# Optimization experiments

Measured on AMD Instinct MI355X. Metric: run time of the kernel, lower is better.

The kernel has to match this reference:

```python
import jax, jax.numpy as jnp
import numpy as np
from jax import lax

B, T, C, K = 16, 1024, 512, 5
PAD = (K - 1) // 2
EPS_LN = 1e-5
EPS_BN = 1e-5


def setup_inputs() -> dict:
    key = jax.random.key(0)
    ks = jax.random.split(key, 8)
    s1 = 1.0 / np.sqrt(C)          # fan-in of pointwise conv1 (C -> 2C)
    s2 = 1.0 / np.sqrt(2 * C * K)  # fan-in of k=5 conv (2C -> 2C)
    s3 = 1.0 / np.sqrt(C)          # fan-in of pointwise conv3 (C -> C)
    return {
        "x": jax.random.normal(ks[0], (B, T, C), jnp.float32),
        "ln_g": jnp.ones((C,), jnp.float32),
        "ln_b": jnp.zeros((C,), jnp.float32),
        "w1": (jax.random.normal(ks[1], (2 * C, C), jnp.float32) * s1),
        "b1": jnp.zeros((2 * C,), jnp.float32),
        "w2": (jax.random.normal(ks[2], (K, 2 * C, 2 * C), jnp.float32) * s2),  # WIO layout
        "b2": jnp.zeros((2 * C,), jnp.float32),
        "bn_g": jnp.ones((C,), jnp.float32),
        "bn_b": jnp.zeros((C,), jnp.float32),
        "bn_mean": jax.random.normal(ks[3], (C,), jnp.float32) * 0.1,
        "bn_var": jax.random.uniform(ks[4], (C,), jnp.float32, 0.5, 1.5),
        "w3": (jax.random.normal(ks[5], (C, C), jnp.float32) * s3),
        "b3": jnp.zeros((C,), jnp.float32),
    }


def reference(x, ln_g, ln_b, w1, b1, w2, b2, bn_g, bn_b, bn_mean, bn_var, w3, b3):
    # LayerNorm over channel dim (B, T, C)
    mu = jnp.mean(x, axis=-1, keepdims=True)
    var = jnp.mean(jnp.square(x - mu), axis=-1, keepdims=True)
    h = (x - mu) * lax.rsqrt(var + EPS_LN) * ln_g + ln_b

    # pointwise conv C -> 2C (kernel 1 == GEMM), then Swish
    h = jnp.einsum('btc,oc->bto', h, w1) + b1        # (B, T, 2C)
    h = h * jax.nn.sigmoid(h)

    # kernel-5 conv 2C -> 2C, 'same' padding, channels-last
    h = lax.conv_general_dilated(
        h, w2, window_strides=(1,), padding=[(PAD, PAD)],
        dimension_numbers=('NWC', 'WIO', 'NWC')) + b2  # (B, T, 2C)

    # GLU over channel dim: first half * sigmoid(second half)
    a, g = h[..., :C], h[..., C:]
    h = a * jax.nn.sigmoid(g)                        # (B, T, C)

    # BatchNorm1d(C), eval mode (running stats)
    h = (h - bn_mean) * lax.rsqrt(bn_var + EPS_BN) * bn_g + bn_b

    # pointwise conv C -> C; dropout is identity at inference.
    # Torch output is sequential(...)(B,C,T).transpose(1,2) -> (B, T, C)
    return jnp.einsum('btc,oc->bto', h, w3) + b3
```

## Files before the change

kernel.cpp:

```cpp
#include <hip/hip_runtime.h>
#include <cstdint>


#define NB    16
#define TT    1024
#define CC    512
#define C2    1024
#define TPAD  1028

typedef unsigned short u16;
typedef short bf16x8 __attribute__((ext_vector_type(8)));
typedef float f32x4  __attribute__((ext_vector_type(4)));
typedef __attribute__((address_space(3))) u16 lds_u16;
typedef const __attribute__((address_space(1))) u16 glb_u16;

__device__ __forceinline__ float bf2f(u16 u) {
  union { unsigned int i; float f; } v; v.i = ((unsigned int)u) << 16; return v.f;
}
__device__ __forceinline__ u16 f2bf(float f) {
  union { float f; unsigned int i; } v; v.f = f;
  unsigned int x = v.i;
  return (u16)((x + 0x7fffu + ((x >> 16) & 1u)) >> 16);
}

__global__ __launch_bounds__(256) void prep_k(
    const float* __restrict__ w1, u16* __restrict__ w1b,
    const float* __restrict__ w3, u16* __restrict__ w3b,
    u16* __restrict__ h1p) {
  const int b = blockIdx.x;
  if (b < 512) {
    const int i = (b * 256 + threadIdx.x) * 4;
    float4 v = *(const float4*)(w1 + i);
    u16 o[4] = { f2bf(v.x), f2bf(v.y), f2bf(v.z), f2bf(v.w) };
    *(uint2*)(w1b + i) = *(const uint2*)o;
  } else if (b < 768) {
    const int i = ((b - 512) * 256 + threadIdx.x) * 4;
    float4 v = *(const float4*)(w3 + i);
    u16 o[4] = { f2bf(v.x), f2bf(v.y), f2bf(v.z), f2bf(v.w) };
    *(uint2*)(w3b + i) = *(const uint2*)o;
  } else {
    const int idx = (b - 768) * 256 + threadIdx.x;
    const int bb  = idx >> 9;
    const int rem = idx & 511;
    const int ri  = rem >> 7;
    const int c8  = (rem & 127) * 8;
    const int row = bb * TPAD + (ri < 2 ? ri : 1024 + ri);
    uint4 z = make_uint4(0u, 0u, 0u, 0u);
    *(uint4*)(h1p + (size_t)row * C2 + c8) = z;
  }
}

__global__ void transpose_w2(const float* __restrict__ w2, u16* __restrict__ w2t) {
  __shared__ u16 t[64][65];
  const int k  = blockIdx.z;
  const int i0 = blockIdx.x * 64, o0 = blockIdx.y * 64;
  const int tx = threadIdx.x, ty = threadIdx.y;
  for (int r = ty; r < 64; r += 4)
    t[r][tx] = f2bf(w2[((size_t)(k * C2) + i0 + r) * C2 + o0 + tx]);
  __syncthreads();
  for (int r = ty; r < 64; r += 4)
    w2t[((size_t)(k * C2) + o0 + r) * C2 + i0 + tx] = t[tx][r];
}

__global__ __launch_bounds__(256) void layernorm_k(
    const float* __restrict__ x, const float* __restrict__ lng,
    const float* __restrict__ lnb, u16* __restrict__ out) {
  const int tok  = blockIdx.x * 4 + (threadIdx.x >> 6);
  const int lane = threadIdx.x & 63;
  const float* xp = x + (size_t)tok * CC + lane * 8;
  float f[8];
  *(float4*)(f)     = *(const float4*)(xp);
  *(float4*)(f + 4) = *(const float4*)(xp + 4);
  float s = 0.f, s2 = 0.f;
#pragma unroll
  for (int j = 0; j < 8; j++) { s += f[j]; s2 += f[j] * f[j]; }
#pragma unroll
  for (int m = 32; m >= 1; m >>= 1) { s += __shfl_xor(s, m, 64); s2 += __shfl_xor(s2, m, 64); }
  const float mu  = s  * (1.f / 512.f);
  const float var = s2 * (1.f / 512.f) - mu * mu;
  const float rs  = rsqrtf(var + 1e-5f);
  u16 ov[8];
#pragma unroll
  for (int j = 0; j < 8; j++) {
    const int c = lane * 8 + j;
    ov[j] = f2bf((f[j] - mu) * rs * lng[c] + lnb[c]);
  }
  *(uint4*)(out + (size_t)tok * CC + lane * 8) = *(const uint4*)ov;
}

template <int EPI>
__global__ __launch_bounds__(256, 3) void gemm_bt(
    const u16* __restrict__ A, const u16* __restrict__ Bt,
    const float* __restrict__ bias, void* __restrict__ outv,
    const int Kd, const int ldA) {
  __shared__ __align__(16) u16 smem[20480];
  const int tid  = threadIdx.x;
  const int m0   = blockIdx.x * 128;
  const int n0   = blockIdx.y * 128;
  const int wave = tid >> 6, lane = tid & 63;
  const int wm = (wave & 1) * 64, wn = (wave >> 1) * 64;
  const int quad = lane >> 4, l16 = lane & 15;
  const int row = tid >> 2;
  const int kc  = (tid & 3) * 8;
  const int J = Kd >> 5;

  const u16* Ap0 = A + (size_t)(m0 + row) * ldA + kc;
  const u16* Ap1 = Ap0 + (size_t)64 * ldA;
  const u16* Bp0 = Bt + (size_t)(n0 + row) * Kd + kc;
  const u16* Bp1 = Bp0 + (size_t)64 * Kd;

  f32x4 acc[4][4] = {};
  uint4 rA0 = *(const uint4*)Ap0, rA1 = *(const uint4*)Ap1;
  uint4 rB0 = *(const uint4*)Bp0, rB1 = *(const uint4*)Bp1;
  *(uint4*)(smem + row * 40 + kc)                = rA0;
  *(uint4*)(smem + (64 + row) * 40 + kc)         = rA1;
  *(uint4*)(smem + 10240 + row * 40 + kc)        = rB0;
  *(uint4*)(smem + 10240 + (64 + row) * 40 + kc) = rB1;
  rA0 = *(const uint4*)(Ap0 + 32); rA1 = *(const uint4*)(Ap1 + 32);
  rB0 = *(const uint4*)(Bp0 + 32); rB1 = *(const uint4*)(Bp1 + 32);
  __syncthreads();

#pragma unroll 1
  for (int j = 0; j < J; j++) {
    const u16* curA = smem + (j & 1) * 5120;
    const u16* curB = smem + 10240 + (j & 1) * 5120;
    if (j + 1 < J) {
      u16* nxtA = smem + ((j + 1) & 1) * 5120;
      u16* nxtB = smem + 10240 + ((j + 1) & 1) * 5120;
      *(uint4*)(nxtA + row * 40 + kc)        = rA0;
      *(uint4*)(nxtA + (64 + row) * 40 + kc) = rA1;
      *(uint4*)(nxtB + row * 40 + kc)        = rB0;
      *(uint4*)(nxtB + (64 + row) * 40 + kc) = rB1;
    }
    {
      const int k2 = (j + 2 < J) ? (j + 2) * 32 : 0;
      rA0 = *(const uint4*)(Ap0 + k2); rA1 = *(const uint4*)(Ap1 + k2);
      rB0 = *(const uint4*)(Bp0 + k2); rB1 = *(const uint4*)(Bp1 + k2);
    }
    bf16x8 af[4], bfr[4];
#pragma unroll
    for (int i = 0; i < 4; i++)
      af[i] = *(const bf16x8*)(curA + (wm + i * 16 + l16) * 40 + quad * 8);
#pragma unroll
    for (int i = 0; i < 4; i++)
      bfr[i] = *(const bf16x8*)(curB + (wn + i * 16 + l16) * 40 + quad * 8);
#pragma unroll
    for (int mi = 0; mi < 4; mi++)
#pragma unroll
      for (int ni = 0; ni < 4; ni++)
        acc[mi][ni] = __builtin_amdgcn_mfma_f32_16x16x32_bf16(
            af[mi], bfr[ni], acc[mi][ni], 0, 0, 0);
    __syncthreads();
  }

  float bv[4];
#pragma unroll
  for (int ni = 0; ni < 4; ni++) bv[ni] = bias[n0 + wn + ni * 16 + l16];

  if (EPI == 0) {
    u16* epi = smem + wave * 4608;
#pragma unroll
    for (int mi = 0; mi < 4; mi++)
#pragma unroll
      for (int ni = 0; ni < 4; ni++)
#pragma unroll
        for (int r = 0; r < 4; r++) {
          float v = acc[mi][ni][r] + bv[ni];
          v = v / (1.f + __expf(-v));
          epi[(mi * 16 + quad * 4 + r) * 72 + ni * 16 + l16] = f2bf(v);
        }
    u16* h1p = (u16*)outv;
#pragma unroll
    for (int p = 0; p < 8; p++) {
      const int rrow = p * 8 + (lane >> 3);
      const int colb = (lane & 7) * 8;
      uint4 v = *(const uint4*)(epi + rrow * 72 + colb);
      const int rr = m0 + wm + rrow;
      const int bb = rr >> 10, tt = rr & 1023;
      *(uint4*)(h1p + (size_t)(bb * TPAD + tt + 2) * C2 + n0 + wn + colb) = v;
    }
  } else {
    float* fepi = (float*)(smem + wave * 4608);
    float* outf = (float*)outv;
#pragma unroll
    for (int mi = 0; mi < 4; mi++) {
      float* fp = fepi + (mi & 1) * 1088;
#pragma unroll
      for (int ni = 0; ni < 4; ni++)
#pragma unroll
        for (int r = 0; r < 4; r++)
          fp[(quad * 4 + r) * 68 + ni * 16 + l16] = acc[mi][ni][r] + bv[ni];
#pragma unroll
      for (int p = 0; p < 4; p++) {
        const int rrow = p * 4 + (lane >> 4);
        const int col  = (lane & 15) * 4;
        float4 v = *(const float4*)(fp + rrow * 68 + col);
        *(float4*)(outf + (size_t)(m0 + wm + mi * 16 + rrow) * CC + n0 + wn + col) = v;
      }
    }
  }
}

__global__ __launch_bounds__(256, 2) void conv5_mfma(
    const u16* __restrict__ h1p, const u16* __restrict__ w2t,
    const float* __restrict__ b2,
    const float* __restrict__ bng, const float* __restrict__ bnb,
    const float* __restrict__ bnm, const float* __restrict__ bnv,
    u16* __restrict__ h2) {
  __shared__ __align__(16) u16 smem[30880];
  const int tid = threadIdx.x;
  const int mt  = blockIdx.x;
  const int ya  = blockIdx.y * 64;
  const int bb  = mt >> 2;
  const int t0  = (mt & 3) * 256;
  const size_t arow0 = (size_t)bb * TPAD + t0;
  const int wave = tid >> 6, lane = tid & 63;
  const int wm = (wave & 1) * 128, wn = (wave >> 1) * 64;
  const int quad = lane >> 4, l16 = lane & 15;
  const int row = tid >> 2;
  const int kc  = (tid & 3) * 8;
  u16* lsB = smem + 10400;

  const u16* Ap0 = h1p + (arow0 + row) * C2 + kc;
  const u16* Ap1 = Ap0 + (size_t)64 * C2;
  const u16* Ap2 = Ap0 + (size_t)128 * C2;
  const u16* Ap3 = Ap0 + (size_t)192 * C2;
  const u16* Ap4 = h1p + (arow0 + 256 + row) * C2 + kc;

  const u16* Bb0 = w2t + (size_t)(ya + wave * 16 + (lane & 15)) * C2 + (lane >> 4) * 8;
  const u16* Bb1 = w2t + (size_t)(512 + ya + wave * 16 + (lane & 15)) * C2 + (lane >> 4) * 8;

  f32x4 acc[8][4] = {};
  uint4 rA0, rA1, rA2, rA3, rA4;

#define BG(PTR, T5, GQ, I0)                                                    \
  __builtin_amdgcn_global_load_lds(                                            \
      (glb_u16*)((PTR) + (size_t)(T5) * C2 * C2 + (I0)),                       \
      (lds_u16*)(lsB + ((T5) * 8 + (GQ)) * 512), 16, 0, 0);

  rA0 = *(const uint4*)Ap0; rA1 = *(const uint4*)Ap1;
  rA2 = *(const uint4*)Ap2; rA3 = *(const uint4*)Ap3;
  if (tid < 16) rA4 = *(const uint4*)Ap4;

#pragma unroll 1
  for (int j = 0; j < 32; j++) {
    __syncthreads();
    {
      const int ib0 = j * 32;
#pragma unroll
      for (int t5 = 0; t5 < 5; t5++) {
        BG(Bb0, t5, wave, ib0)
        BG(Bb1, t5, wave + 4, ib0)
      }
    }
    *(uint4*)(smem + row * 40 + kc)         = rA0;
    *(uint4*)(smem + (64 + row) * 40 + kc)  = rA1;
    *(uint4*)(smem + (128 + row) * 40 + kc) = rA2;
    *(uint4*)(smem + (192 + row) * 40 + kc) = rA3;
    if (tid < 16) *(uint4*)(smem + (256 + row) * 40 + kc) = rA4;
    __syncthreads();
    {
      const int ia = (j + 1 < 32) ? (j + 1) * 32 : 0;
      rA0 = *(const uint4*)(Ap0 + ia);
      rA1 = *(const uint4*)(Ap1 + ia);
      rA2 = *(const uint4*)(Ap2 + ia);
      rA3 = *(const uint4*)(Ap3 + ia);
      if (tid < 16) rA4 = *(const uint4*)(Ap4 + ia);
    }
#pragma unroll
    for (int k = 0; k < 5; k++) {
      bf16x8 bfr[4];
#pragma unroll
      for (int i = 0; i < 4; i++)
        bfr[i] = *(const bf16x8*)(lsB + (k * 8 + (wn >> 4) + i) * 512 + lane * 8);
#pragma unroll
      for (int h = 0; h < 2; h++) {
        bf16x8 af[4];
#pragma unroll
        for (int i = 0; i < 4; i++)
          af[i] = *(const bf16x8*)(smem + (wm + (h * 4 + i) * 16 + l16 + k) * 40 + quad * 8);
#pragma unroll
        for (int mi = 0; mi < 4; mi++)
#pragma unroll
          for (int ni = 0; ni < 4; ni++)
            acc[h * 4 + mi][ni] = __builtin_amdgcn_mfma_f32_16x16x32_bf16(
                af[mi], bfr[ni], acc[h * 4 + mi][ni], 0, 0, 0);
      }
    }
  }
#undef BG
  __syncthreads();

  float bv[4];
#pragma unroll
  for (int ni = 0; ni < 4; ni++)
    bv[ni] = b2[(wn >> 6) * 512 + ya + ni * 16 + l16];

  const int cb8 = (lane & 7) * 8;
  float sc8[8], bm8[8], bb8[8];
#pragma unroll
  for (int jj = 0; jj < 8; jj++) {
    const int c = ya + cb8 + jj;
    sc8[jj] = bng[c] * rsqrtf(bnv[c] + 1e-5f);
    bm8[jj] = bnm[c];
    bb8[jj] = bnb[c];
  }

  u16* abuf = smem;
  u16* gbuf = smem + 9216;
  const size_t orow0 = (size_t)bb * TT + t0;
#pragma unroll 1
  for (int hh = 0; hh < 2; hh++) {
    if ((wave & 1) == hh) {
      u16* buf = (wn >> 6) ? gbuf : abuf;
#pragma unroll
      for (int mi = 0; mi < 8; mi++)
#pragma unroll
        for (int ni = 0; ni < 4; ni++)
#pragma unroll
          for (int r = 0; r < 4; r++)
            buf[(mi * 16 + quad * 4 + r) * 72 + ni * 16 + l16] =
                f2bf(acc[mi][ni][r] + bv[ni]);
    }
    __syncthreads();
#pragma unroll
    for (int p = 0; p < 4; p++) {
      const int rr = wave * 32 + p * 8 + (lane >> 3);
      uint4 va = *(const uint4*)(abuf + rr * 72 + cb8);
      uint4 vg = *(const uint4*)(gbuf + rr * 72 + cb8);
      u16 aa[8], gg[8], oo[8];
      *(uint4*)aa = va; *(uint4*)gg = vg;
#pragma unroll
      for (int jj = 0; jj < 8; jj++) {
        const float a = bf2f(aa[jj]);
        const float g = bf2f(gg[jj]);
        const float h = a / (1.f + __expf(-g));
        oo[jj] = f2bf((h - bm8[jj]) * sc8[jj] + bb8[jj]);
      }
      *(uint4*)(h2 + (orow0 + hh * 128 + rr) * CC + ya + cb8) = *(const uint4*)oo;
    }
    __syncthreads();
  }
}

extern "C" void kernel_launch(void* const* d_in, const int* in_sizes, int n_in,
                              void* d_out, int out_size, void* d_ws, size_t ws_size,
                              hipStream_t stream) {
  const float* x   = (const float*)d_in[0];
  const float* lng = (const float*)d_in[1];
  const float* lnb = (const float*)d_in[2];
  const float* w1  = (const float*)d_in[3];
  const float* b1  = (const float*)d_in[4];
  const float* w2  = (const float*)d_in[5];
  const float* b2  = (const float*)d_in[6];
  const float* bng = (const float*)d_in[7];
  const float* bnb = (const float*)d_in[8];
  const float* bnm = (const float*)d_in[9];
  const float* bnv = (const float*)d_in[10];
  const float* w3  = (const float*)d_in[11];
  const float* b3  = (const float*)d_in[12];

  u16* ws  = (u16*)d_ws;
  u16* hln = ws;
  u16* h2  = hln;
  u16* h1p = ws + 8388608;
  u16* w2t = h1p + 16842752;
  u16* hcv = w2t + 5242880;
  u16* w1b = hcv + 16777216;
  u16* w3b = w1b + 524288;

  prep_k      <<<800, 256, 0, stream>>>(w1, w1b, w3, w3b, h1p);
  transpose_w2<<<dim3(16, 16, 5), dim3(64, 4), 0, stream>>>(w2, w2t);
  layernorm_k <<<4096, 256, 0, stream>>>(x, lng, lnb, hln);
  gemm_bt<0>  <<<dim3(128, 8), 256, 0, stream>>>(hln, w1b, b1, h1p, 512, 512);
  conv5_mfma  <<<dim3(64, 8), 256, 0, stream>>>(h1p, w2t, b2, bng, bnb, bnm, bnv, h2);
  gemm_bt<1>  <<<dim3(128, 4), 256, 0, stream>>>(h2, w3b, b3, d_out, 512, 512);
}
```

Measured before the change: 310.3 us.

## Merge prep, w2 transpose and layernorm into one launch; add dedicated SiLU GEMM

After: 312.7 us. About the same (+0.8%).

```diff
diff --git a/kernel.cpp b/kernel.cpp
--- a/kernel.cpp
+++ b/kernel.cpp
@@ -23,23 +23,28 @@
   return (u16)((x + 0x7fffu + ((x >> 16) & 1u)) >> 16);
 }
 
-__global__ __launch_bounds__(256) void prep_k(
+__global__ __launch_bounds__(256) void preproc_k(
     const float* __restrict__ w1, u16* __restrict__ w1b,
     const float* __restrict__ w3, u16* __restrict__ w3b,
-    u16* __restrict__ h1p) {
-  const int b = blockIdx.x;
+    u16* __restrict__ h1p,
+    const float* __restrict__ w2, u16* __restrict__ w2t,
+    const float* __restrict__ x, const float* __restrict__ lng,
+    const float* __restrict__ lnb, u16* __restrict__ hln) {
+  __shared__ u16 t[64][65];
+  const int b   = blockIdx.x;
+  const int tid = threadIdx.x;
   if (b < 512) {
-    const int i = (b * 256 + threadIdx.x) * 4;
+    const int i = (b * 256 + tid) * 4;
     float4 v = *(const float4*)(w1 + i);
     u16 o[4] = { f2bf(v.x), f2bf(v.y), f2bf(v.z), f2bf(v.w) };
     *(uint2*)(w1b + i) = *(const uint2*)o;
   } else if (b < 768) {
-    const int i = ((b - 512) * 256 + threadIdx.x) * 4;
+    const int i = ((b - 512) * 256 + tid) * 4;
     float4 v = *(const float4*)(w3 + i);
     u16 o[4] = { f2bf(v.x), f2bf(v.y), f2bf(v.z), f2bf(v.w) };
     *(uint2*)(w3b + i) = *(const uint2*)o;
-  } else {
-    const int idx = (b - 768) * 256 + threadIdx.x;
+  } else if (b < 800) {
+    const int idx = (b - 768) * 256 + tid;
     const int bb  = idx >> 9;
     const int rem = idx & 511;
     const int ri  = rem >> 7;
@@ -47,45 +52,145 @@
     const int row = bb * TPAD + (ri < 2 ? ri : 1024 + ri);
     uint4 z = make_uint4(0u, 0u, 0u, 0u);
     *(uint4*)(h1p + (size_t)row * C2 + c8) = z;
-  }
-}
-
-__global__ void transpose_w2(const float* __restrict__ w2, u16* __restrict__ w2t) {
-  __shared__ u16 t[64][65];
-  const int k  = blockIdx.z;
-  const int i0 = blockIdx.x * 64, o0 = blockIdx.y * 64;
-  const int tx = threadIdx.x, ty = threadIdx.y;
-  for (int r = ty; r < 64; r += 4)
-    t[r][tx] = f2bf(w2[((size_t)(k * C2) + i0 + r) * C2 + o0 + tx]);
+  } else if (b < 2080) {
+    const int bt = b - 800;
+    const int k  = bt >> 8;
+    const int rem = bt & 255;
+    const int i0 = (rem & 15) * 64, o0 = (rem >> 4) * 64;
+    const int tx = tid & 63, ty = tid >> 6;
+    for (int r = ty; r < 64; r += 4)
+      t[r][tx] = f2bf(w2[((size_t)(k * C2) + i0 + r) * C2 + o0 + tx]);
+    __syncthreads();
+    for (int r = ty; r < 64; r += 4)
+      w2t[((size_t)(k * C2) + o0 + r) * C2 + i0 + tx] = t[tx][r];
+  } else {
+    const int tok  = (b - 2080) * 4 + (tid >> 6);
+    const int lane = tid & 63;
+    const float* xp = x + (size_t)tok * CC + lane * 8;
+    float f[8];
+    *(float4*)(f)     = *(const float4*)(xp);
+    *(float4*)(f + 4) = *(const float4*)(xp + 4);
+    float s = 0.f, s2 = 0.f;
+#pragma unroll
+    for (int j = 0; j < 8; j++) { s += f[j]; s2 += f[j] * f[j]; }
+#pragma unroll
+    for (int m = 32; m >= 1; m >>= 1) { s += __shfl_xor(s, m, 64); s2 += __shfl_xor(s2, m, 64); }
+    const float mu  = s  * (1.f / 512.f);
+    const float var = s2 * (1.f / 512.f) - mu * mu;
+    const float rs  = rsqrtf(var + 1e-5f);
+    u16 ov[8];
+#pragma unroll
+    for (int j = 0; j < 8; j++) {
+      const int c = lane * 8 + j;
+      ov[j] = f2bf((f[j] - mu) * rs * lng[c] + lnb[c]);
+    }
+    *(uint4*)(hln + (size_t)tok * CC + lane * 8) = *(const uint4*)ov;
+  }
+}
+
+__global__ __launch_bounds__(256, 2) void gemm0_silu(
+    const u16* __restrict__ hln, const u16* __restrict__ w1b,
+    const float* __restrict__ b1, u16* __restrict__ h1p) {
+  __shared__ __align__(16) u16 smem[18432];
+  const int tid = threadIdx.x;
+  const int mt  = blockIdx.x;
+  const int n0  = blockIdx.y * 128;
+  const int m0  = mt * 256;
+  const int bb  = mt >> 2;
+  const int t0  = (mt & 3) * 256;
+  const int wave = tid >> 6, lane = tid & 63;
+  const int wm = (wave & 1) * 128, wn = (wave >> 1) * 64;
+  const int quad = lane >> 4, l16 = lane & 15;
+  const int row = tid >> 2;
+  const int kc  = (tid & 3) * 8;
+  u16* lsB = smem + 10240;
+
+  const u16* Ap0 = hln + (size_t)(m0 + row) * CC + kc;
+  const u16* Ap1 = Ap0 + (size_t)64 * CC;
+  const u16* Ap2 = Ap0 + (size_t)128 * CC;
+  const u16* Ap3 = Ap0 + (size_t)192 * CC;
+
+  const u16* Bb0 = w1b + (size_t)(n0 + wave * 16 + (lane & 15)) * CC + (lane >> 4) * 8;
+  const u16* Bb1 = Bb0 + (size_t)64 * CC;
+
+  f32x4 acc[8][4] = {};
+  uint4 rA0, rA1, rA2, rA3;
+
+#define BG0(PTR, GQ, I0)                                                       \
+  __builtin_amdgcn_global_load_lds(                                            \
+      (glb_u16*)((PTR) + (I0)),                                                \
+      (lds_u16*)(lsB + (GQ) * 512), 16, 0, 0);
+
+  rA0 = *(const uint4*)Ap0; rA1 = *(const uint4*)Ap1;
+  rA2 = *(const uint4*)Ap2; rA3 = *(const uint4*)Ap3;
+
+#pragma unroll 1
+  for (int j = 0; j < 16; j++) {
+    __syncthreads();
+    {
+      const int jb = j * 32;
+      BG0(Bb0, wave, jb)
+      BG0(Bb1, wave + 4, jb)
+    }
+    *(uint4*)(smem + row * 40 + kc)         = rA0;
+    *(uint4*)(smem + (64 + row) * 40 + kc)  = rA1;
+    *(uint4*)(smem + (128 + row) * 40 + kc) = rA2;
+    *(uint4*)(smem + (192 + row) * 40 + kc) = rA3;
+    __syncthreads();
+    {
+      const int ia = (j + 1 < 16) ? (j + 1) * 32 : 0;
+      rA0 = *(const uint4*)(Ap0 + ia);
+      rA1 = *(const uint4*)(Ap1 + ia);
+      rA2 = *(const uint4*)(Ap2 + ia);
+      rA3 = *(const uint4*)(Ap3 + ia);
+    }
+    bf16x8 bfr[4];
+#pragma unroll
+    for (int i = 0; i < 4; i++)
+      bfr[i] = *(const bf16x8*)(lsB + ((wn >> 4) + i) * 512 + lane * 8);
+#pragma unroll
+    for (int h = 0; h < 2; h++) {
+      bf16x8 af[4];
+#pragma unroll
+      for (int i = 0; i < 4; i++)
+        af[i] = *(const bf16x8*)(smem + (wm + (h * 4 + i) * 16 + l16) * 40 + quad * 8);
+#pragma unroll
+      for (int mi = 0; mi < 4; mi++)
+#pragma unroll
+        for (int ni = 0; ni < 4; ni++)
+          acc[h * 4 + mi][ni] = __builtin_amdgcn_mfma_f32_16x16x32_bf16(
+              af[mi], bfr[ni], acc[h * 4 + mi][ni], 0, 0, 0);
+    }
+  }
+#undef BG0
   __syncthreads();
-  for (int r = ty; r < 64; r += 4)
-    w2t[((size_t)(k * C2) + o0 + r) * C2 + i0 + tx] = t[tx][r];
-}
-
-__global__ __launch_bounds__(256) void layernorm_k(
-    const float* __restrict__ x, const float* __restrict__ lng,
-    const float* __restrict__ lnb, u16* __restrict__ out) {
-  const int tok  = blockIdx.x * 4 + (threadIdx.x >> 6);
-  const int lane = threadIdx.x & 63;
-  const float* xp = x + (size_t)tok * CC + lane * 8;
-  float f[8];
-  *(float4*)(f)     = *(const float4*)(xp);
-  *(float4*)(f + 4) = *(const float4*)(xp + 4);
-  float s = 0.f, s2 = 0.f;
-#pragma unroll
-  for (int j = 0; j < 8; j++) { s += f[j]; s2 += f[j] * f[j]; }
-#pragma unroll
-  for (int m = 32; m >= 1; m >>= 1) { s += __shfl_xor(s, m, 64); s2 += __shfl_xor(s2, m, 64); }
-  const float mu  = s  * (1.f / 512.f);
-  const float var = s2 * (1.f / 512.f) - mu * mu;
-  const float rs  = rsqrtf(var + 1e-5f);
-  u16 ov[8];
-#pragma unroll
-  for (int j = 0; j < 8; j++) {
-    const int c = lane * 8 + j;
-    ov[j] = f2bf((f[j] - mu) * rs * lng[c] + lnb[c]);
-  }
-  *(uint4*)(out + (size_t)tok * CC + lane * 8) = *(const uint4*)ov;
+
+  float bv[4];
+#pragma unroll
+  for (int ni = 0; ni < 4; ni++) bv[ni] = b1[n0 + wn + ni * 16 + l16];
+
+  u16* epi = smem + wave * 4608;
+#pragma unroll
+  for (int h = 0; h < 2; h++) {
+#pragma unroll
+    for (int mi = 0; mi < 4; mi++)
+#pragma unroll
+      for (int ni = 0; ni < 4; ni++)
+#pragma unroll
+        for (int r = 0; r < 4; r++) {
+          float v = acc[h * 4 + mi][ni][r] + bv[ni];
+          v = v / (1.f + __expf(-v));
+          epi[(mi * 16 + quad * 4 + r) * 72 + ni * 16 + l16] = f2bf(v);
+        }
+#pragma unroll
+    for (int p = 0; p < 8; p++) {
+      const int rrow = p * 8 + (lane >> 3);
+      const int colb = (lane & 7) * 8;
+      uint4 v = *(const uint4*)(epi + rrow * 72 + colb);
+      const int tt = t0 + wm + h * 64 + rrow;
+      *(uint4*)(h1p + (size_t)(bb * TPAD + tt + 2) * C2 + n0 + wn + colb) = v;
+    }
+  }
 }
 
 template <int EPI>
@@ -369,10 +474,9 @@
   u16* w1b = hcv + 16777216;
   u16* w3b = w1b + 524288;
 
-  prep_k      <<<800, 256, 0, stream>>>(w1, w1b, w3, w3b, h1p);
-  transpose_w2<<<dim3(16, 16, 5), dim3(64, 4), 0, stream>>>(w2, w2t);
-  layernorm_k <<<4096, 256, 0, stream>>>(x, lng, lnb, hln);
-  gemm_bt<0>  <<<dim3(128, 8), 256, 0, stream>>>(hln, w1b, b1, h1p, 512, 512);
-  conv5_mfma  <<<dim3(64, 8), 256, 0, stream>>>(h1p, w2t, b2, bng, bnb, bnm, bnv, h2);
-  gemm_bt<1>  <<<dim3(128, 4), 256, 0, stream>>>(h2, w3b, b3, d_out, 512, 512);
-}
+  preproc_k  <<<6176, 256, 0, stream>>>(w1, w1b, w3, w3b, h1p, w2, w2t,
+                                        x, lng, lnb, hln);
+  gemm0_silu <<<dim3(64, 8), 256, 0, stream>>>(hln, w1b, b1, h1p);
+  conv5_mfma <<<dim3(64, 8), 256, 0, stream>>>(h1p, w2t, b2, bng, bnb, bnm, bnv, h2);
+  gemm_bt<1> <<<dim3(128, 4), 256, 0, stream>>>(h2, w3b, b3, d_out, 512, 512);
+}
```
